# Kernel optimization log

Hardware: AMD Instinct MI355X
Metric: run time of the kernel (lower is better)

Reference implementation:

```python
import jax, jax.numpy as jnp
import numpy as np

D_MODEL = 512
NHEAD = 8
HEAD_DIM = D_MODEL // NHEAD  # 64
ROTARY_DIM = HEAD_DIM        # rotary_dim defaults to head_dim
WINDOW = (127, 128)          # (left, right) sliding window, flash-attn convention
ROPE_BASE = 10000.0


def setup_inputs() -> dict:
    key = jax.random.key(0)
    k1, k2, k3, k4 = jax.random.split(key, 4)
    N, T = 4, 2048
    x = jax.random.normal(k1, (N, T, D_MODEL), dtype=jnp.float32)
    # Wqkv: Linear(d_model, 3*d_model, bias=False) -> weight [3*D, D]
    Wqkv_w = jax.random.normal(k2, (3 * D_MODEL, D_MODEL), dtype=jnp.float32) * (D_MODEL ** -0.5)
    # out_proj: Linear(d_model, d_model, bias=True)
    out_w = jax.random.normal(k3, (D_MODEL, D_MODEL), dtype=jnp.float32) * (D_MODEL ** -0.5)
    out_b = jax.random.normal(k4, (D_MODEL,), dtype=jnp.float32) * 0.01
    return {"x": x, "Wqkv_w": Wqkv_w, "out_w": out_w, "out_b": out_b}


def _rope_cos_sin(T, dtype):
    # flash-attn RotaryEmbedding: inv_freq over even indices of rotary_dim
    inv_freq = 1.0 / (ROPE_BASE ** (jnp.arange(0, ROTARY_DIM, 2, dtype=jnp.float32) / ROTARY_DIM))
    t = jnp.arange(T, dtype=jnp.float32)
    freqs = jnp.outer(t, inv_freq)  # [T, ROTARY_DIM//2]
    return jnp.cos(freqs).astype(dtype), jnp.sin(freqs).astype(dtype)


def _apply_rotary(x, cos, sin):
    # non-interleaved (rotate halves); x: [N, T, H, hd], rotary over first ROTARY_DIM dims
    r, rest = x[..., :ROTARY_DIM], x[..., ROTARY_DIM:]
    half = ROTARY_DIM // 2
    x1, x2 = r[..., :half], r[..., half:]
    c = cos[None, :, None, :]  # [1, T, 1, half]
    s = sin[None, :, None, :]
    rotated = jnp.concatenate([x1 * c - x2 * s, x2 * c + x1 * s], axis=-1)
    return jnp.concatenate([rotated, rest], axis=-1) if rest.shape[-1] else rotated


def reference(x, Wqkv_w, out_w, out_b):
    N, T, D = x.shape
    qkv = jnp.einsum('ntd,ed->nte', x, Wqkv_w).reshape(N, T, 3, NHEAD, HEAD_DIM)
    q, k, v = qkv[:, :, 0], qkv[:, :, 1], qkv[:, :, 2]  # each [N, T, H, hd]
    cos, sin = _rope_cos_sin(T, x.dtype)
    q = _apply_rotary(q, cos, sin)
    k = _apply_rotary(k, cos, sin)
    scale = HEAD_DIM ** -0.5
    scores = jnp.einsum('nthd,nshd->nhts', q, k) * scale  # [N, H, T, T]
    # sliding window: query i attends key j iff i - left <= j <= i + right
    i = jnp.arange(T)[:, None]
    j = jnp.arange(T)[None, :]
    mask = (j >= i - WINDOW[0]) & (j <= i + WINDOW[1])  # [T, T]
    scores = jnp.where(mask[None, None], scores, jnp.finfo(scores.dtype).min)
    attn = jax.nn.softmax(scores, axis=-1)
    ctx = jnp.einsum('nhts,nshd->nthd', attn, v).reshape(N, T, D)
    return jnp.einsum('ntd,ed->nte', ctx, out_w) + out_b
```

## Files before the change

### kernel.cpp

```cpp
#include <hip/hip_runtime.h>
#include <math.h>

#define TSEQ 2048
#define NB 4
#define DM 512
#define NH 8
#define HD 64

typedef _Float16 half8 __attribute__((ext_vector_type(8)));
typedef _Float16 half4 __attribute__((ext_vector_type(4)));
typedef float floatx4 __attribute__((ext_vector_type(4)));

#if __has_builtin(__builtin_amdgcn_exp2f)
#define EXP2F(x) __builtin_amdgcn_exp2f(x)
#else
#define EXP2F(x) exp2f(x)
#endif

__device__ __forceinline__ void gl2lds16(const _Float16* g, _Float16* l) {
  const __attribute__((address_space(1))) unsigned int* gp =
      (const __attribute__((address_space(1))) unsigned int*)(uintptr_t)g;
  __attribute__((address_space(3))) unsigned int* lp =
      (__attribute__((address_space(3))) unsigned int*)(uintptr_t)l;
  __builtin_amdgcn_global_load_lds(gp, lp, 16, 0, 0);
}


#define WS_END_U16 2916352

__global__ void prep(const float* __restrict__ x, const float* __restrict__ wqkv,
                     const float* __restrict__ ow, char* __restrict__ ws) {
  for (int i = blockIdx.x * 256 + threadIdx.x; i < WS_END_U16; i += 2048 * 256) {
    if (i < 524288) {
      const float4 a = ((const float4*)x)[2 * i];
      const float4 b = ((const float4*)x)[2 * i + 1];
      half8 h;
      h[0] = (_Float16)a.x; h[1] = (_Float16)a.y; h[2] = (_Float16)a.z; h[3] = (_Float16)a.w;
      h[4] = (_Float16)b.x; h[5] = (_Float16)b.y; h[6] = (_Float16)b.z; h[7] = (_Float16)b.w;
      *(half8*)(ws + (size_t)i * 16) = h;
    } else if (i >= 540672 && i < 638976) {
      const int o = i - 540672;
      const float4 a = ((const float4*)wqkv)[2 * o];
      const float4 b = ((const float4*)wqkv)[2 * o + 1];
      half8 h;
      h[0] = (_Float16)a.x; h[1] = (_Float16)a.y; h[2] = (_Float16)a.z; h[3] = (_Float16)a.w;
      h[4] = (_Float16)b.x; h[5] = (_Float16)b.y; h[6] = (_Float16)b.z; h[7] = (_Float16)b.w;
      *(half8*)(ws + (size_t)i * 16) = h;
    } else if (i >= 655360 && i < 688128) {
      const int o = i - 655360;
      const float4 a = ((const float4*)ow)[2 * o];
      const float4 b = ((const float4*)ow)[2 * o + 1];
      half8 h;
      h[0] = (_Float16)a.x; h[1] = (_Float16)a.y; h[2] = (_Float16)a.z; h[3] = (_Float16)a.w;
      h[4] = (_Float16)b.x; h[5] = (_Float16)b.y; h[6] = (_Float16)b.z; h[7] = (_Float16)b.w;
      *(half8*)(ws + (size_t)i * 16) = h;
    } else if (i >= 2883584) {
      const int u = i - 2883584;
      float4 o4;
      {
        const int id = 2 * u, t = id >> 5, fi = id & 31;
        const float invf = powf(10000.0f, -(float)(2 * fi) * (1.0f / 64.0f));
        float s, c; sincosf((float)t * invf, &s, &c);
        o4.x = c; o4.y = s;
      }
      {
        const int id = 2 * u + 1, t = id >> 5, fi = id & 31;
        const float invf = powf(10000.0f, -(float)(2 * fi) * (1.0f / 64.0f));
        float s, c; sincosf((float)t * invf, &s, &c);
        o4.z = c; o4.w = s;
      }
      ((float4*)(ws + 46137344))[u] = o4;
    } else {
      ((float4*)ws)[i] = make_float4(0.f, 0.f, 0.f, 0.f);
    }
  }
}

__global__ __launch_bounds__(256) void qkv_gemm_mfma(
    const _Float16* __restrict__ A, const _Float16* __restrict__ B,
    const float2* __restrict__ rope,
    _Float16* __restrict__ qb, _Float16* __restrict__ kb, _Float16* __restrict__ vT)
{
  __shared__ __align__(16) _Float16 As[128 * 32];
  __shared__ __align__(16) _Float16 Bs[128 * 32];
  const int tid = threadIdx.x;
  const int wv = tid >> 6, lane = tid & 63, quad = lane >> 4, col = lane & 15;
  const int wm = wv >> 1, we = wv & 1;
  const int m0 = blockIdx.x << 7, c0 = blockIdx.y << 7;
  const int r0 = tid >> 2, p0 = tid & 3;
  const int cA0 = (p0 - (r0 >> 1)) & 3;
  const int r1 = (tid + 256) >> 2, p1 = tid & 3;
  const int cA1 = (p1 - (r1 >> 1)) & 3;
  const _Float16* ga0 = &A[(size_t)(m0 + r0) * DM + cA0 * 8];
  const _Float16* ga1 = &A[(size_t)(m0 + r1) * DM + cA1 * 8];
  const _Float16* gb0 = &B[(size_t)(c0 + r0) * DM + cA0 * 8];
  const _Float16* gb1 = &B[(size_t)(c0 + r1) * DM + cA1 * 8];
  _Float16* la0 = &As[tid * 8];
  _Float16* la1 = &As[(tid + 256) * 8];
  _Float16* lb0 = &Bs[tid * 8];
  _Float16* lb1 = &Bs[(tid + 256) * 8];
  floatx4 acc[4][4] = {};
  for (int k0 = 0; k0 < DM; k0 += 32) {
    __syncthreads();
    gl2lds16(ga0 + k0, la0);
    gl2lds16(ga1 + k0, la1);
    gl2lds16(gb0 + k0, lb0);
    gl2lds16(gb1 + k0, lb1);
    __syncthreads();
    half8 af[4], bf[4];
#pragma unroll
    for (int mt = 0; mt < 4; mt++) {
      const int R = wm * 64 + mt * 16 + col;
      af[mt] = *(const half8*)&As[R * 32 + (((quad + (R >> 1)) & 3) << 3)];
    }
#pragma unroll
    for (int et = 0; et < 4; et++) {
      const int R = we * 64 + et * 16 + col;
      bf[et] = *(const half8*)&Bs[R * 32 + (((quad + (R >> 1)) & 3) << 3)];
    }
#pragma unroll
    for (int mt = 0; mt < 4; mt++)
#pragma unroll
      for (int et = 0; et < 4; et++)
        acc[mt][et] = __builtin_amdgcn_mfma_f32_16x16x32_f16(af[mt], bf[et], acc[mt][et], 0, 0, 0);
  }
  const int eidx = (c0 >> 6) + we;
  const int three = eidx >> 3, h = eidx & 7;
  const int mbase = m0 + wm * 64 + quad * 4;
  if (three == 2) {
#pragma unroll
    for (int mt = 0; mt < 4; mt++) {
      const int m = mbase + mt * 16;
      const int n = m >> 11, t = m & 2047;
#pragma unroll
      for (int et = 0; et < 4; et++) {
        const int dh = et * 16 + col;
        half4 hv;
#pragma unroll
        for (int r = 0; r < 4; r++) hv[r] = (_Float16)acc[mt][et][r];
        *(half4*)&vT[(size_t)(n * NH + h) * HD * TSEQ + (size_t)dh * TSEQ + t] = hv;
      }
    }
  } else {
    _Float16* dst = three ? kb : qb;
    const float scl = three ? 1.0f : 0.125f * 1.4426950408889634f;
#pragma unroll
    for (int mt = 0; mt < 4; mt++)
#pragma unroll
      for (int r = 0; r < 4; r++) {
        const int m = mbase + mt * 16 + r;
        const int n = m >> 11, t = m & 2047;
#pragma unroll
        for (int et = 0; et < 4; et++) {
          const int i = ((et & 1) << 4) + col;
          const float2 cs = rope[t * 32 + i];
          const float v = acc[mt][et][r];
          const float v2 = acc[mt][et ^ 2][r];
          const float o = (et < 2) ? (v * cs.x - v2 * cs.y) : (v * cs.x + v2 * cs.y);
          dst[((size_t)(n * NH + h) * TSEQ + t) * HD + et * 16 + col] = (_Float16)(o * scl);
        }
      }
  }
}

__global__ __launch_bounds__(256, 4) void attn_win_mfma(
    const _Float16* __restrict__ qb, const _Float16* __restrict__ kb,
    const _Float16* __restrict__ vT, _Float16* __restrict__ ctx)
{
  __shared__ __align__(16) char smem[36864];
  _Float16* Ks = (_Float16*)smem;
  _Float16* Vt = (_Float16*)(smem + 9216);
  _Float16* Ps = (_Float16*)(smem + 18432);
  _Float16* Osh = (_Float16*)(smem + 27648);

  const int tid = threadIdx.x;
  const int wv = tid >> 6;
  const int lane = tid & 63;
  const int quad = lane >> 4;
  const int col = lane & 15;
  const int nh = blockIdx.y;
  const int q0 = blockIdx.x << 6;
  const _Float16* qp = qb + (size_t)nh * TSEQ * HD;
  const _Float16* kp = kb + (size_t)nh * TSEQ * HD;
  const _Float16* vp = vT + (size_t)nh * HD * TSEQ;

  const int i_row = (wv << 4) + col;
  const int ig = q0 + i_row;
  const half8 qf0 = *(const half8*)&qp[(size_t)ig * HD + (quad << 3)];
  const half8 qf1 = *(const half8*)&qp[(size_t)ig * HD + 32 + (quad << 3)];

  float l_i = 0.0f;
  floatx4 accO[4] = {};

  const int kt0 = max(0, q0 - 127) >> 6;
  const int kt1 = min(TSEQ - 1, q0 + 191) >> 6;
  const int kr = tid >> 2, kc = (tid & 3) << 4;
  const int vd = tid >> 2, vc = (tid & 3) << 4;
  for (int kt = kt0; kt <= kt1; kt++) {
    const int j0 = kt << 6;
    const half8 k0_ = *(const half8*)&kp[(size_t)(j0 + kr) * HD + kc];
    const half8 k1_ = *(const half8*)&kp[(size_t)(j0 + kr) * HD + kc + 8];
    const half8 v0_ = *(const half8*)&vp[(size_t)vd * TSEQ + j0 + vc];
    const half8 v1_ = *(const half8*)&vp[(size_t)vd * TSEQ + j0 + vc + 8];
    __syncthreads();
    *(half8*)&Ks[kr * 72 + kc] = k0_;
    *(half8*)&Ks[kr * 72 + kc + 8] = k1_;
    *(half8*)&Vt[vd * 72 + vc] = v0_;
    *(half8*)&Vt[vd * 72 + vc + 8] = v1_;
    __syncthreads();

    floatx4 S[4];
#pragma unroll
    for (int js = 0; js < 4; js++) {
      const half8 a0 = *(const half8*)&Ks[((js << 4) + col) * 72 + (quad << 3)];
      const half8 a1 = *(const half8*)&Ks[((js << 4) + col) * 72 + 32 + (quad << 3)];
      floatx4 c = {0.f, 0.f, 0.f, 0.f};
      c = __builtin_amdgcn_mfma_f32_16x16x32_f16(a0, qf0, c, 0, 0, 0);
      c = __builtin_amdgcn_mfma_f32_16x16x32_f16(a1, qf1, c, 0, 0, 0);
      S[js] = c;
    }
#pragma unroll
    for (int js = 0; js < 4; js++) {
      half4 ph;
#pragma unroll
      for (int r = 0; r < 4; r++) {
        const int jg = j0 + (js << 4) + (quad << 2) + r;
        const bool valid = (jg >= ig - 127) && (jg <= ig + 128);
        const float p = valid ? EXP2F(S[js][r]) : 0.0f;
        l_i += p;
        ph[r] = (_Float16)p;
      }
      *(half4*)&Ps[i_row * 72 + (js << 4) + (quad << 2)] = ph;
    }
    const half8 pa0 = *(const half8*)&Ps[i_row * 72 + (quad << 3)];
    const half8 pa1 = *(const half8*)&Ps[i_row * 72 + 32 + (quad << 3)];
#pragma unroll
    for (int d4 = 0; d4 < 4; d4++) {
      const half8 vb0 = *(const half8*)&Vt[((d4 << 4) + col) * 72 + (quad << 3)];
      const half8 vb1 = *(const half8*)&Vt[((d4 << 4) + col) * 72 + 32 + (quad << 3)];
      accO[d4] = __builtin_amdgcn_mfma_f32_16x16x32_f16(pa0, vb0, accO[d4], 0, 0, 0);
      accO[d4] = __builtin_amdgcn_mfma_f32_16x16x32_f16(pa1, vb1, accO[d4], 0, 0, 0);
    }
  }
  l_i += __shfl_xor(l_i, 16, 64);
  l_i += __shfl_xor(l_i, 32, 64);
  {
    const float linv = 1.0f / l_i;
    float l4[4];
#pragma unroll
    for (int r = 0; r < 4; r++) l4[r] = __shfl(linv, (quad << 2) + r, 64);
#pragma unroll
    for (int d4 = 0; d4 < 4; d4++)
#pragma unroll
      for (int r = 0; r < 4; r++)
        Osh[((wv << 4) + (quad << 2) + r) * 72 + (d4 << 4) + col] = (_Float16)(accO[d4][r] * l4[r]);
  }
  __syncthreads();
  {
    const int n = nh >> 3, h = nh & 7;
    const int oi = tid >> 2, oc = (tid & 3) << 4;
    _Float16* dst = &ctx[((size_t)n * TSEQ + q0 + oi) * DM + h * HD + oc];
    *(half8*)&dst[0] = *(const half8*)&Osh[oi * 72 + oc];
    *(half8*)&dst[8] = *(const half8*)&Osh[oi * 72 + oc + 8];
  }
}

__global__ __launch_bounds__(256) void out_gemm_mfma(
    const _Float16* __restrict__ A, const _Float16* __restrict__ B,
    const float* __restrict__ bias, float* __restrict__ out)
{
  __shared__ _Float16 As[128 * 40];
  __shared__ _Float16 Bs[64 * 40];
  const int tid = threadIdx.x;
  const int wv = tid >> 6, lane = tid & 63, quad = lane >> 4, col = lane & 15;
  const int wm = wv >> 1, we = wv & 1;
  const int m0 = blockIdx.x << 7, c0 = blockIdx.y << 6;
  const int sr = tid >> 1, sc = (tid & 1) << 4;
  const int br = tid >> 2, bc = (tid & 3) << 3;
  const _Float16* ap = &A[(size_t)(m0 + sr) * DM + sc];
  const _Float16* bp = &B[(size_t)(c0 + br) * DM + bc];
  floatx4 acc[4][2] = {};
  for (int k0 = 0; k0 < DM; k0 += 32) {
    const half8 a0 = *(const half8*)(ap + k0);
    const half8 a1 = *(const half8*)(ap + k0 + 8);
    const half8 b0 = *(const half8*)(bp + k0);
    __syncthreads();
    *(half8*)&As[sr * 40 + sc] = a0;
    *(half8*)&As[sr * 40 + sc + 8] = a1;
    *(half8*)&Bs[br * 40 + bc] = b0;
    __syncthreads();
    half8 af[4], bf[2];
#pragma unroll
    for (int mt = 0; mt < 4; mt++)
      af[mt] = *(const half8*)&As[(wm * 64 + mt * 16 + col) * 40 + quad * 8];
#pragma unroll
    for (int et = 0; et < 2; et++)
      bf[et] = *(const half8*)&Bs[(we * 32 + et * 16 + col) * 40 + quad * 8];
#pragma unroll
    for (int mt = 0; mt < 4; mt++)
#pragma unroll
      for (int et = 0; et < 2; et++)
        acc[mt][et] = __builtin_amdgcn_mfma_f32_16x16x32_f16(af[mt], bf[et], acc[mt][et], 0, 0, 0);
  }
  float bb[2];
#pragma unroll
  for (int et = 0; et < 2; et++) bb[et] = bias[c0 + we * 32 + et * 16 + col];
  const int mbase = m0 + wm * 64 + quad * 4;
#pragma unroll
  for (int mt = 0; mt < 4; mt++)
#pragma unroll
    for (int r = 0; r < 4; r++) {
      const int m = mbase + mt * 16 + r;
#pragma unroll
      for (int et = 0; et < 2; et++)
        out[(size_t)m * DM + c0 + we * 32 + et * 16 + col] = acc[mt][et][r] + bb[et];
    }
}

extern "C" void kernel_launch(void* const* d_in, const int* in_sizes, int n_in,
                              void* d_out, int out_size, void* d_ws, size_t ws_size,
                              hipStream_t stream) {
  const float* x    = (const float*)d_in[0];
  const float* wqkv = (const float*)d_in[1];
  const float* ow   = (const float*)d_in[2];
  const float* ob   = (const float*)d_in[3];
  char* ws = (char*)d_ws;
  _Float16* xh    = (_Float16*)(ws);
  _Float16* wqkvh = (_Float16*)(ws + 8650752);
  _Float16* owh   = (_Float16*)(ws + 10485760);
  _Float16* qbuf  = (_Float16*)(ws + 11534336);
  _Float16* kbuf  = (_Float16*)(ws + 20971520);
  _Float16* vTb   = (_Float16*)(ws + 29360128);
  _Float16* ctxh  = (_Float16*)(ws + 37748736);
  float2*   rope  = (float2*)  (ws + 46137344);

  prep<<<2048, 256, 0, stream>>>(x, wqkv, ow, ws);
  qkv_gemm_mfma<<<dim3(64, 12), 256, 0, stream>>>(xh, wqkvh, rope, qbuf, kbuf, vTb);
  attn_win_mfma<<<dim3(32, 32), 256, 0, stream>>>(qbuf, kbuf, vTb, ctxh);
  out_gemm_mfma<<<dim3(64, 8), 256, 0, stream>>>(ctxh, owh, ob, (float*)d_out);
}
```

Baseline: 135.2 us.

## Fuse fp32-to-fp16 conversion into GEMM loads, drop prep conversion pass

```diff
diff --git a/kernel.cpp b/kernel.cpp
--- a/kernel.cpp
+++ b/kernel.cpp
@@ -17,45 +17,16 @@
 #define EXP2F(x) exp2f(x)
 #endif
 
-__device__ __forceinline__ void gl2lds16(const _Float16* g, _Float16* l) {
-  const __attribute__((address_space(1))) unsigned int* gp =
-      (const __attribute__((address_space(1))) unsigned int*)(uintptr_t)g;
-  __attribute__((address_space(3))) unsigned int* lp =
-      (__attribute__((address_space(3))) unsigned int*)(uintptr_t)l;
-  __builtin_amdgcn_global_load_lds(gp, lp, 16, 0, 0);
-}
-
-
-#define WS_END_U16 2916352
-
-__global__ void prep(const float* __restrict__ x, const float* __restrict__ wqkv,
-                     const float* __restrict__ ow, char* __restrict__ ws) {
-  for (int i = blockIdx.x * 256 + threadIdx.x; i < WS_END_U16; i += 2048 * 256) {
-    if (i < 524288) {
-      const float4 a = ((const float4*)x)[2 * i];
-      const float4 b = ((const float4*)x)[2 * i + 1];
-      half8 h;
-      h[0] = (_Float16)a.x; h[1] = (_Float16)a.y; h[2] = (_Float16)a.z; h[3] = (_Float16)a.w;
-      h[4] = (_Float16)b.x; h[5] = (_Float16)b.y; h[6] = (_Float16)b.z; h[7] = (_Float16)b.w;
-      *(half8*)(ws + (size_t)i * 16) = h;
-    } else if (i >= 540672 && i < 638976) {
-      const int o = i - 540672;
-      const float4 a = ((const float4*)wqkv)[2 * o];
-      const float4 b = ((const float4*)wqkv)[2 * o + 1];
-      half8 h;
-      h[0] = (_Float16)a.x; h[1] = (_Float16)a.y; h[2] = (_Float16)a.z; h[3] = (_Float16)a.w;
-      h[4] = (_Float16)b.x; h[5] = (_Float16)b.y; h[6] = (_Float16)b.z; h[7] = (_Float16)b.w;
-      *(half8*)(ws + (size_t)i * 16) = h;
-    } else if (i >= 655360 && i < 688128) {
-      const int o = i - 655360;
-      const float4 a = ((const float4*)ow)[2 * o];
-      const float4 b = ((const float4*)ow)[2 * o + 1];
-      half8 h;
-      h[0] = (_Float16)a.x; h[1] = (_Float16)a.y; h[2] = (_Float16)a.z; h[3] = (_Float16)a.w;
-      h[4] = (_Float16)b.x; h[5] = (_Float16)b.y; h[6] = (_Float16)b.z; h[7] = (_Float16)b.w;
-      *(half8*)(ws + (size_t)i * 16) = h;
-    } else if (i >= 2883584) {
-      const int u = i - 2883584;
+
+#define PREP_LO_U16 720896
+#define ROPE_U16    2883584
+#define WS_END_U16  2916352
+
+__global__ void prep(char* __restrict__ ws) {
+  for (int i = PREP_LO_U16 + blockIdx.x * 256 + threadIdx.x; i < WS_END_U16;
+       i += 2048 * 256) {
+    if (i >= ROPE_U16) {
+      const int u = i - ROPE_U16;
       float4 o4;
       {
         const int id = 2 * u, t = id >> 5, fi = id & 31;
@@ -69,55 +40,55 @@
         float s, c; sincosf((float)t * invf, &s, &c);
         o4.z = c; o4.w = s;
       }
-      ((float4*)(ws + 46137344))[u] = o4;
+      ((float4*)ws)[i] = o4;
     } else {
       ((float4*)ws)[i] = make_float4(0.f, 0.f, 0.f, 0.f);
     }
   }
 }
 
+__device__ __forceinline__ half8 cvt8(const float* p) {
+  const float4 a = *(const float4*)p;
+  const float4 b = *(const float4*)(p + 4);
+  half8 h;
+  h[0] = (_Float16)a.x; h[1] = (_Float16)a.y; h[2] = (_Float16)a.z; h[3] = (_Float16)a.w;
+  h[4] = (_Float16)b.x; h[5] = (_Float16)b.y; h[6] = (_Float16)b.z; h[7] = (_Float16)b.w;
+  return h;
+}
+
 __global__ __launch_bounds__(256) void qkv_gemm_mfma(
-    const _Float16* __restrict__ A, const _Float16* __restrict__ B,
+    const float* __restrict__ A, const float* __restrict__ B,
     const float2* __restrict__ rope,
     _Float16* __restrict__ qb, _Float16* __restrict__ kb, _Float16* __restrict__ vT)
 {
-  __shared__ __align__(16) _Float16 As[128 * 32];
-  __shared__ __align__(16) _Float16 Bs[128 * 32];
+  __shared__ _Float16 As[128 * 40];
+  __shared__ _Float16 Bs[128 * 40];
   const int tid = threadIdx.x;
   const int wv = tid >> 6, lane = tid & 63, quad = lane >> 4, col = lane & 15;
   const int wm = wv >> 1, we = wv & 1;
   const int m0 = blockIdx.x << 7, c0 = blockIdx.y << 7;
-  const int r0 = tid >> 2, p0 = tid & 3;
-  const int cA0 = (p0 - (r0 >> 1)) & 3;
-  const int r1 = (tid + 256) >> 2, p1 = tid & 3;
-  const int cA1 = (p1 - (r1 >> 1)) & 3;
-  const _Float16* ga0 = &A[(size_t)(m0 + r0) * DM + cA0 * 8];
-  const _Float16* ga1 = &A[(size_t)(m0 + r1) * DM + cA1 * 8];
-  const _Float16* gb0 = &B[(size_t)(c0 + r0) * DM + cA0 * 8];
-  const _Float16* gb1 = &B[(size_t)(c0 + r1) * DM + cA1 * 8];
-  _Float16* la0 = &As[tid * 8];
-  _Float16* la1 = &As[(tid + 256) * 8];
-  _Float16* lb0 = &Bs[tid * 8];
-  _Float16* lb1 = &Bs[(tid + 256) * 8];
+  const int sr = tid >> 1, sc = (tid & 1) << 4;
+  const float* ap = &A[(size_t)(m0 + sr) * DM + sc];
+  const float* bp = &B[(size_t)(c0 + sr) * DM + sc];
   floatx4 acc[4][4] = {};
   for (int k0 = 0; k0 < DM; k0 += 32) {
-    __syncthreads();
-    gl2lds16(ga0 + k0, la0);
-    gl2lds16(ga1 + k0, la1);
-    gl2lds16(gb0 + k0, lb0);
-    gl2lds16(gb1 + k0, lb1);
+    const half8 a0 = cvt8(ap + k0);
+    const half8 a1 = cvt8(ap + k0 + 8);
+    const half8 b0 = cvt8(bp + k0);
+    const half8 b1 = cvt8(bp + k0 + 8);
+    __syncthreads();
+    *(half8*)&As[sr * 40 + sc] = a0;
+    *(half8*)&As[sr * 40 + sc + 8] = a1;
+    *(half8*)&Bs[sr * 40 + sc] = b0;
+    *(half8*)&Bs[sr * 40 + sc + 8] = b1;
     __syncthreads();
     half8 af[4], bf[4];
 #pragma unroll
-    for (int mt = 0; mt < 4; mt++) {
-      const int R = wm * 64 + mt * 16 + col;
-      af[mt] = *(const half8*)&As[R * 32 + (((quad + (R >> 1)) & 3) << 3)];
-    }
-#pragma unroll
-    for (int et = 0; et < 4; et++) {
-      const int R = we * 64 + et * 16 + col;
-      bf[et] = *(const half8*)&Bs[R * 32 + (((quad + (R >> 1)) & 3) << 3)];
-    }
+    for (int mt = 0; mt < 4; mt++)
+      af[mt] = *(const half8*)&As[(wm * 64 + mt * 16 + col) * 40 + quad * 8];
+#pragma unroll
+    for (int et = 0; et < 4; et++)
+      bf[et] = *(const half8*)&Bs[(we * 64 + et * 16 + col) * 40 + quad * 8];
 #pragma unroll
     for (int mt = 0; mt < 4; mt++)
 #pragma unroll
@@ -266,7 +237,7 @@
 }
 
 __global__ __launch_bounds__(256) void out_gemm_mfma(
-    const _Float16* __restrict__ A, const _Float16* __restrict__ B,
+    const _Float16* __restrict__ A, const float* __restrict__ B,
     const float* __restrict__ bias, float* __restrict__ out)
 {
   __shared__ _Float16 As[128 * 40];
@@ -278,12 +249,12 @@
   const int sr = tid >> 1, sc = (tid & 1) << 4;
   const int br = tid >> 2, bc = (tid & 3) << 3;
   const _Float16* ap = &A[(size_t)(m0 + sr) * DM + sc];
-  const _Float16* bp = &B[(size_t)(c0 + br) * DM + bc];
+  const float* bp = &B[(size_t)(c0 + br) * DM + bc];
   floatx4 acc[4][2] = {};
   for (int k0 = 0; k0 < DM; k0 += 32) {
     const half8 a0 = *(const half8*)(ap + k0);
     const half8 a1 = *(const half8*)(ap + k0 + 8);
-    const half8 b0 = *(const half8*)(bp + k0);
+    const half8 b0 = cvt8(bp + k0);
     __syncthreads();
     *(half8*)&As[sr * 40 + sc] = a0;
     *(half8*)&As[sr * 40 + sc + 8] = a1;
@@ -325,17 +296,14 @@
   const float* ow   = (const float*)d_in[2];
   const float* ob   = (const float*)d_in[3];
   char* ws = (char*)d_ws;
-  _Float16* xh    = (_Float16*)(ws);
-  _Float16* wqkvh = (_Float16*)(ws + 8650752);
-  _Float16* owh   = (_Float16*)(ws + 10485760);
   _Float16* qbuf  = (_Float16*)(ws + 11534336);
   _Float16* kbuf  = (_Float16*)(ws + 20971520);
   _Float16* vTb   = (_Float16*)(ws + 29360128);
   _Float16* ctxh  = (_Float16*)(ws + 37748736);
   float2*   rope  = (float2*)  (ws + 46137344);
 
-  prep<<<2048, 256, 0, stream>>>(x, wqkv, ow, ws);
-  qkv_gemm_mfma<<<dim3(64, 12), 256, 0, stream>>>(xh, wqkvh, rope, qbuf, kbuf, vTb);
+  prep<<<2048, 256, 0, stream>>>(ws);
+  qkv_gemm_mfma<<<dim3(64, 12), 256, 0, stream>>>(x, wqkv, rope, qbuf, kbuf, vTb);
   attn_win_mfma<<<dim3(32, 32), 256, 0, stream>>>(qbuf, kbuf, vTb, ctxh);
-  out_gemm_mfma<<<dim3(64, 8), 256, 0, stream>>>(ctxh, owh, ob, (float*)d_out);
-}
+  out_gemm_mfma<<<dim3(64, 8), 256, 0, stream>>>(ctxh, ow, ob, (float*)d_out);
+}
```

New measurement: 151.9 us. 12.4% more time.
